# Kernel tuning notes

Hardware: AMD Instinct MI355X
Metric: run time of the kernel (lower is better)

## Reference

```python
import jax, jax.numpy as jnp
import numpy as np

N_PROP = 1000
N_CLS = 81  # includes background class 0
IMG_H, IMG_W = 800, 1333
WX, WY, WW, WH = 10.0, 10.0, 5.0, 5.0
BBOX_XFORM_CLIP = float(np.log(1000.0 / 16.0))
SCORE_THRESH = 0.05
NMS_THRESH = 0.5
DET_PER_IMG = 100


def _decode(box_regression, proposals):
    widths = proposals[:, 2] - proposals[:, 0] + 1.0
    heights = proposals[:, 3] - proposals[:, 1] + 1.0
    ctr_x = proposals[:, 0] + 0.5 * widths
    ctr_y = proposals[:, 1] + 0.5 * heights
    rel = box_regression.reshape(box_regression.shape[0], -1, 4)  # [N, C, 4]
    dx = rel[..., 0] / WX
    dy = rel[..., 1] / WY
    dw = jnp.minimum(rel[..., 2] / WW, BBOX_XFORM_CLIP)
    dh = jnp.minimum(rel[..., 3] / WH, BBOX_XFORM_CLIP)
    pcx = dx * widths[:, None] + ctr_x[:, None]
    pcy = dy * heights[:, None] + ctr_y[:, None]
    pw = jnp.exp(dw) * widths[:, None]
    ph = jnp.exp(dh) * heights[:, None]
    return jnp.stack([pcx - 0.5 * pw, pcy - 0.5 * ph,
                      pcx + 0.5 * pw - 1.0, pcy + 0.5 * ph - 1.0], axis=-1)  # [N, C, 4]


def _clip_boxes(b, h, w):
    x1 = jnp.clip(b[..., 0], 0.0, w - 1.0)
    y1 = jnp.clip(b[..., 1], 0.0, h - 1.0)
    x2 = jnp.clip(b[..., 2], 0.0, w - 1.0)
    y2 = jnp.clip(b[..., 3], 0.0, h - 1.0)
    return jnp.stack([x1, y1, x2, y2], axis=-1)


def _nms_keep(boxes, scores, valid):
    # Greedy NMS for one class. boxes [N,4], scores [N], valid [N].
    # Returns keep mask in the ORIGINAL proposal order.
    n = scores.shape[0]
    order = jnp.argsort(-jnp.where(valid, scores, -jnp.inf))
    b = boxes[order]
    v = valid[order]
    x1, y1, x2, y2 = b[:, 0], b[:, 1], b[:, 2], b[:, 3]
    area = (x2 - x1 + 1.0) * (y2 - y1 + 1.0)
    iw = jnp.clip(jnp.minimum(x2[:, None], x2[None, :]) - jnp.maximum(x1[:, None], x1[None, :]) + 1.0, 0.0)
    ih = jnp.clip(jnp.minimum(y2[:, None], y2[None, :]) - jnp.maximum(y1[:, None], y1[None, :]) + 1.0, 0.0)
    inter = iw * ih
    iou = inter / (area[:, None] + area[None, :] - inter)
    idx = jnp.arange(n)

    def body(i, keep):
        sup = (iou[i] > NMS_THRESH) & (idx > i) & keep[i]
        return keep & ~sup

    keep = jax.lax.fori_loop(0, n, body, v)
    return jnp.zeros(n, dtype=bool).at[order].set(keep)


def _postprocess(class_logits, box_regression, proposal_boxes, image_h, image_w):
    prob = jax.nn.softmax(class_logits, axis=-1)             # [N, C]
    boxes = _decode(box_regression, proposal_boxes)           # [N, C, 4]
    boxes = _clip_boxes(boxes, float(image_h), float(image_w))
    scores_c = prob[:, 1:].T                                  # [C-1, N] skip background
    boxes_c = jnp.transpose(boxes[:, 1:, :], (1, 0, 2))       # [C-1, N, 4]
    valid = scores_c > SCORE_THRESH
    keep = jax.vmap(_nms_keep)(boxes_c, scores_c, valid)      # [C-1, N]
    masked = jnp.where(keep, scores_c, -jnp.inf)
    count = jnp.sum(keep)
    # torch.kthvalue(n - 100) == 101st largest kept score; keep scores >= it
    topv = jax.lax.top_k(masked.reshape(-1), DET_PER_IMG + 1)[0]
    image_thresh = jnp.where(count > DET_PER_IMG, topv[DET_PER_IMG], -jnp.inf)
    final = keep & (masked >= image_thresh)
    c1, n = scores_c.shape
    labels = jnp.broadcast_to(jnp.arange(1, c1 + 1, dtype=jnp.int32)[:, None], (c1, n))
    out_scores = jnp.where(final, scores_c, 0.0).reshape(-1)
    out_boxes = jnp.where(final[..., None], boxes_c, 0.0).reshape(-1, 4)
    out5 = jnp.concatenate([out_boxes, out_scores[:, None]], axis=1)  # [(C-1)*N, 5]
    return out5, jnp.where(final, labels, 0).reshape(-1), final.reshape(-1)


def setup_inputs() -> dict:
    key = jax.random.key(0)
    k1, k2, k3, k4 = jax.random.split(key, 4)
    # scale logits so a realistic fraction of softmax scores clears the 0.05 threshold
    class_logits = 3.0 * jax.random.normal(k1, (N_PROP, N_CLS), dtype=jnp.float32)
    box_regression = jax.random.normal(k2, (N_PROP, N_CLS * 4), dtype=jnp.float32)
    cxy = jax.random.uniform(k3, (N_PROP, 2), dtype=jnp.float32) * jnp.array([IMG_W, IMG_H], jnp.float32)
    wh = 16.0 + 284.0 * jax.random.uniform(k4, (N_PROP, 2), dtype=jnp.float32)
    x1y1 = jnp.clip(cxy - 0.5 * wh, 0.0)
    x2y2 = jnp.minimum(cxy + 0.5 * wh, jnp.array([IMG_W - 1.0, IMG_H - 1.0], jnp.float32))
    proposal_boxes = jnp.concatenate([x1y1, x2y2], axis=1)  # [N, 4] xyxy
    return {"class_logits": class_logits, "box_regression": box_regression,
            "proposal_boxes": proposal_boxes, "image_h": IMG_H, "image_w": IMG_W}


def reference(class_logits, box_regression, proposal_boxes, image_h, image_w):
    return _postprocess(class_logits, box_regression, proposal_boxes, image_h, image_w)
```

## Files before the change

kernel.cpp:

```cpp
#include <hip/hip_runtime.h>
#include <math.h>

#define N_PROP 1000
#define N_CLS  81
#define N_FG   80
#define SCORE_THRESH 0.05f
#define NMS_THRESH   0.5f
#define DET_PER_IMG  100
#define BBOX_CLIP    4.135166556742356f

#define LBL_OFF    400000
#define FIN_OFF    480000


__global__ __launch_bounds__(256)
void softmax_zero_kernel(const float* __restrict__ logits,
                         float* __restrict__ out,
                         int* __restrict__ count,
                         float* __restrict__ probT) {
    const int b = blockIdx.x;
    const int t = threadIdx.x;
    const int lane = t & 63;
    const int wave = t >> 6;
    if (b == 0 && t == 0) *count = 0;

    float4 z = make_float4(0.f, 0.f, 0.f, 0.f);
    float4* o4 = (float4*)out;
    for (int i = b * 256 + t; i < 140000; i += 250 * 256) o4[i] = z;

    const int n = b * 4 + wave;
    if (n < N_PROP) {
        const float* lrow = logits + (size_t)n * N_CLS;
        float v0 = lrow[lane];
        float v1 = (lane + 64 < N_CLS) ? lrow[lane + 64] : -INFINITY;
        float m = fmaxf(v0, v1);
        for (int off = 32; off; off >>= 1) m = fmaxf(m, __shfl_down(m, off));
        m = __shfl(m, 0);
        float e0 = expf(v0 - m);
        float e1 = (lane + 64 < N_CLS) ? expf(v1 - m) : 0.0f;
        float s = e0 + e1;
        for (int off = 32; off; off >>= 1) s += __shfl_down(s, off);
        s = __shfl(s, 0);
        if (lane >= 1)          probT[(size_t)(lane - 1) * N_PROP + n] = e0 / s;
        if (lane + 64 < N_CLS)  probT[(size_t)(lane + 63) * N_PROP + n] = e1 / s;
    }
}

__global__ __launch_bounds__(256)
void nms_kernel(const float* __restrict__ probT,
                const float* __restrict__ props,
                const float* __restrict__ reg,
                const int* __restrict__ ihp,
                const int* __restrict__ iwp,
                float* __restrict__ out,
                int* __restrict__ count,
                float* __restrict__ compact,
                int* __restrict__ svRow) {
    const int c = blockIdx.x;
    const int t = threadIdx.x;
    const int lane = t & 63;
    const int cls = c + 1;
    const unsigned long long lm = (1ull << lane) - 1ull;

    __shared__ float sSc[N_PROP];
    __shared__ int   sIdx[N_PROP];
    __shared__ int   sPos[N_PROP];
    __shared__ float sx1[N_PROP], sy1[N_PROP], sx2[N_PROP], sy2[N_PROP];
    __shared__ float sar[N_PROP], sSc2[N_PROP];
    __shared__ int   sJdx[N_PROP];
    __shared__ unsigned char sKeep[N_PROP];
    __shared__ int   shV;

    for (int j = t; j < N_PROP; j += 256) sSc[j] = probT[(size_t)c * N_PROP + j];
    __syncthreads();

    if (t < 64) {
        int V = 0;
        #pragma unroll
        for (int it = 0; it < 16; ++it) {
            int j = it * 64 + lane;
            float sc = (j < N_PROP) ? sSc[j] : -1.0f;
            bool val = (j < N_PROP) && (sc > SCORE_THRESH);
            unsigned long long mask = __ballot(val);
            if (val) { int p = V + __popcll(mask & lm); sSc[p] = sc; sIdx[p] = j; }
            V += __popcll(mask);
        }
        if (lane == 0) shV = V;
    }
    __syncthreads();
    const int V = shV;

    for (int v = t; v < V; v += 256) {
        float s = sSc[v];
        int id = sIdx[v];
        int r = 0;
        for (int u = 0; u < V; ++u) {
            float su = sSc[u];
            r += (su > s) || (su == s && sIdx[u] < id);
        }
        sPos[v] = r;
    }
    __syncthreads();

    const float W1 = (float)iwp[0] - 1.0f;
    const float H1 = (float)ihp[0] - 1.0f;
    for (int v = t; v < V; v += 256) {
        int r = sPos[v];
        int j = sIdx[v];
        float4 pr = *(const float4*)(props + (size_t)j * 4);
        float w  = pr.z - pr.x + 1.0f;
        float h  = pr.w - pr.y + 1.0f;
        float cx = pr.x + 0.5f * w;
        float cy = pr.y + 0.5f * h;
        float4 rr = *(const float4*)(reg + ((size_t)j * N_CLS + cls) * 4);
        float dx = rr.x / 10.0f;
        float dy = rr.y / 10.0f;
        float dw = fminf(rr.z / 5.0f, BBOX_CLIP);
        float dh = fminf(rr.w / 5.0f, BBOX_CLIP);
        float pcx = dx * w + cx;
        float pcy = dy * h + cy;
        float pw = expf(dw) * w;
        float ph = expf(dh) * h;
        float bx1 = pcx - 0.5f * pw;
        float by1 = pcy - 0.5f * ph;
        float bx2 = pcx + 0.5f * pw - 1.0f;
        float by2 = pcy + 0.5f * ph - 1.0f;
        bx1 = fminf(fmaxf(bx1, 0.0f), W1);
        bx2 = fminf(fmaxf(bx2, 0.0f), W1);
        by1 = fminf(fmaxf(by1, 0.0f), H1);
        by2 = fminf(fmaxf(by2, 0.0f), H1);
        sx1[r] = bx1; sy1[r] = by1; sx2[r] = bx2; sy2[r] = by2;
        sar[r] = (bx2 - bx1 + 1.0f) * (by2 - by1 + 1.0f);
        sSc2[r] = sSc[v];
        sJdx[r] = j;
        sKeep[r] = 1;
    }
    __syncthreads();

    for (int r = 0; r < V; ++r) {
        if (sKeep[r]) {
            const float X1 = sx1[r], Y1 = sy1[r], X2 = sx2[r], Y2 = sy2[r], A = sar[r];
            for (int v = r + 1 + t; v < V; v += 256) {
                if (sKeep[v]) {
                    float iw = fminf(X2, sx2[v]) - fmaxf(X1, sx1[v]) + 1.0f;
                    float ih = fminf(Y2, sy2[v]) - fmaxf(Y1, sy1[v]) + 1.0f;
                    iw = fmaxf(iw, 0.0f);
                    ih = fmaxf(ih, 0.0f);
                    float inter = iw * ih;
                    float iou = inter / (A + sar[v] - inter);
                    if (iou > NMS_THRESH) sKeep[v] = 0;
                }
            }
        }
        __syncthreads();
    }

    for (int vb = 0; vb < V; vb += 256) {
        int v = vb + t;
        bool k = (v < V) && sKeep[v];
        unsigned long long mask = __ballot(k);
        int cntw = __popcll(mask);
        int base = 0;
        if (lane == 0 && cntw > 0) base = atomicAdd(count, cntw);
        base = __shfl(base, 0);
        if (k) {
            int row = c * N_PROP + sJdx[v];
            size_t o = (size_t)row * 5;
            out[o + 0] = sx1[v];
            out[o + 1] = sy1[v];
            out[o + 2] = sx2[v];
            out[o + 3] = sy2[v];
            out[o + 4] = sSc2[v];
            out[LBL_OFF + row] = (float)cls;
            out[FIN_OFF + row] = 1.0f;
            int pos = base + __popcll(mask & lm);
            compact[pos] = sSc2[v];
            svRow[pos] = row;
        }
    }
}

__global__ __launch_bounds__(256)
void finalize_kernel(float* __restrict__ out,
                     const float* __restrict__ compact,
                     const int* __restrict__ svRow,
                     const int* __restrict__ count) {
    __shared__ float lsc[8192];
    __shared__ float sTh;
    const int n = *count;
    const int t = threadIdx.x;
    const int lane = t & 63;

    if (n <= DET_PER_IMG) return;

    const bool useL = (n <= 8192);
    if (useL) {
        for (int i = t; i < n; i += 256) lsc[i] = compact[i];
    }
    __syncthreads();

    if (t < 64) {
        unsigned lo = 0x3D4CCCCCu, hi = 0x40000000u;
        while (hi - lo > 1u) {
            unsigned mid = lo + ((hi - lo) >> 1);
            float mv = __uint_as_float(mid);
            int cnt = 0;
            if (useL) {
                for (int i = lane; i < n; i += 64) cnt += (lsc[i] >= mv) ? 1 : 0;
            } else {
                for (int i = lane; i < n; i += 64) cnt += (compact[i] >= mv) ? 1 : 0;
            }
            for (int off = 32; off; off >>= 1) cnt += __shfl_xor(cnt, off);
            if (cnt >= DET_PER_IMG + 1) lo = mid; else hi = mid;
        }
        if (lane == 0) sTh = __uint_as_float(lo);
    }
    __syncthreads();
    const float th = sTh;

    for (int i = blockIdx.x * 256 + t; i < n; i += gridDim.x * 256) {
        float sc = compact[i];
        if (sc < th) {
            int row = svRow[i];
            size_t o = (size_t)row * 5;
            out[o + 0] = 0.0f;
            out[o + 1] = 0.0f;
            out[o + 2] = 0.0f;
            out[o + 3] = 0.0f;
            out[o + 4] = 0.0f;
            out[LBL_OFF + row] = 0.0f;
            out[FIN_OFF + row] = 0.0f;
        }
    }
}

extern "C" void kernel_launch(void* const* d_in, const int* in_sizes, int n_in,
                              void* d_out, int out_size, void* d_ws, size_t ws_size,
                              hipStream_t stream) {
    const float* logits = (const float*)d_in[0];
    const float* reg    = (const float*)d_in[1];
    const float* props  = (const float*)d_in[2];
    const int*   ihp    = (const int*)d_in[3];
    const int*   iwp    = (const int*)d_in[4];
    float* out = (float*)d_out;

    char* ws = (char*)d_ws;
    int*   count   = (int*)(ws + 0);
    float* probT   = (float*)(ws + 64);
    float* compact = (float*)(ws + 320064);
    int*   svRow   = (int*)(ws + 640064);

    softmax_zero_kernel<<<250, 256, 0, stream>>>(logits, out, count, probT);
    nms_kernel<<<N_FG, 256, 0, stream>>>(probT, props, reg, ihp, iwp,
                                         out, count, compact, svRow);
    finalize_kernel<<<16, 256, 0, stream>>>(out, compact, svRow, count);
}
```

Baseline: 70.28 us.

## Add bitmask-based single-wave NMS fast path for classes with at most 128 candidates

For classes with at most 128 candidates above the score threshold, the kernel now fuses rank computation with box decoding. It precomputes a per-box suppression bitmask against all higher-ranked boxes, then runs greedy NMS inside a single wave using ballots instead of one block-wide barrier per candidate. This removes up to V __syncthreads in the serial NMS loop. The cost is a full triangular IoU computation, done without early skipping of already suppressed boxes. Larger classes fall back to the original path.

```diff
diff --git a/kernel.cpp b/kernel.cpp
--- a/kernel.cpp
+++ b/kernel.cpp
@@ -69,6 +69,7 @@
     __shared__ float sar[N_PROP], sSc2[N_PROP];
     __shared__ int   sJdx[N_PROP];
     __shared__ unsigned char sKeep[N_PROP];
+    __shared__ unsigned long long sColMask[128][2];
     __shared__ int   shV;
 
     for (int j = t; j < N_PROP; j += 256) sSc[j] = probT[(size_t)c * N_PROP + j];
@@ -90,92 +91,190 @@
     __syncthreads();
     const int V = shV;
 
-    for (int v = t; v < V; v += 256) {
-        float s = sSc[v];
-        int id = sIdx[v];
-        int r = 0;
-        for (int u = 0; u < V; ++u) {
-            float su = sSc[u];
-            r += (su > s) || (su == s && sIdx[u] < id);
-        }
-        sPos[v] = r;
-    }
-    __syncthreads();
-
     const float W1 = (float)iwp[0] - 1.0f;
     const float H1 = (float)ihp[0] - 1.0f;
-    for (int v = t; v < V; v += 256) {
-        int r = sPos[v];
-        int j = sIdx[v];
-        float4 pr = *(const float4*)(props + (size_t)j * 4);
-        float w  = pr.z - pr.x + 1.0f;
-        float h  = pr.w - pr.y + 1.0f;
-        float cx = pr.x + 0.5f * w;
-        float cy = pr.y + 0.5f * h;
-        float4 rr = *(const float4*)(reg + ((size_t)j * N_CLS + cls) * 4);
-        float dx = rr.x / 10.0f;
-        float dy = rr.y / 10.0f;
-        float dw = fminf(rr.z / 5.0f, BBOX_CLIP);
-        float dh = fminf(rr.w / 5.0f, BBOX_CLIP);
-        float pcx = dx * w + cx;
-        float pcy = dy * h + cy;
-        float pw = expf(dw) * w;
-        float ph = expf(dh) * h;
-        float bx1 = pcx - 0.5f * pw;
-        float by1 = pcy - 0.5f * ph;
-        float bx2 = pcx + 0.5f * pw - 1.0f;
-        float by2 = pcy + 0.5f * ph - 1.0f;
-        bx1 = fminf(fmaxf(bx1, 0.0f), W1);
-        bx2 = fminf(fmaxf(bx2, 0.0f), W1);
-        by1 = fminf(fmaxf(by1, 0.0f), H1);
-        by2 = fminf(fmaxf(by2, 0.0f), H1);
-        sx1[r] = bx1; sy1[r] = by1; sx2[r] = bx2; sy2[r] = by2;
-        sar[r] = (bx2 - bx1 + 1.0f) * (by2 - by1 + 1.0f);
-        sSc2[r] = sSc[v];
-        sJdx[r] = j;
-        sKeep[r] = 1;
-    }
-    __syncthreads();
-
-    for (int r = 0; r < V; ++r) {
-        if (sKeep[r]) {
-            const float X1 = sx1[r], Y1 = sy1[r], X2 = sx2[r], Y2 = sy2[r], A = sar[r];
-            for (int v = r + 1 + t; v < V; v += 256) {
-                if (sKeep[v]) {
-                    float iw = fminf(X2, sx2[v]) - fmaxf(X1, sx1[v]) + 1.0f;
-                    float ih = fminf(Y2, sy2[v]) - fmaxf(Y1, sy1[v]) + 1.0f;
-                    iw = fmaxf(iw, 0.0f);
-                    ih = fmaxf(ih, 0.0f);
-                    float inter = iw * ih;
-                    float iou = inter / (A + sar[v] - inter);
-                    if (iou > NMS_THRESH) sKeep[v] = 0;
+
+    if (V <= 128) {
+        if (t < V) {
+            float s = sSc[t];
+            int id = sIdx[t];
+            int r = 0;
+            for (int u = 0; u < V; ++u) {
+                float su = sSc[u];
+                r += (su > s) || (su == s && sIdx[u] < id);
+            }
+            float4 pr = *(const float4*)(props + (size_t)id * 4);
+            float w  = pr.z - pr.x + 1.0f;
+            float h  = pr.w - pr.y + 1.0f;
+            float cx = pr.x + 0.5f * w;
+            float cy = pr.y + 0.5f * h;
+            float4 rr = *(const float4*)(reg + ((size_t)id * N_CLS + cls) * 4);
+            float dx = rr.x / 10.0f;
+            float dy = rr.y / 10.0f;
+            float dw = fminf(rr.z / 5.0f, BBOX_CLIP);
+            float dh = fminf(rr.w / 5.0f, BBOX_CLIP);
+            float pcx = dx * w + cx;
+            float pcy = dy * h + cy;
+            float pw = expf(dw) * w;
+            float ph = expf(dh) * h;
+            float bx1 = fminf(fmaxf(pcx - 0.5f * pw, 0.0f), W1);
+            float by1 = fminf(fmaxf(pcy - 0.5f * ph, 0.0f), H1);
+            float bx2 = fminf(fmaxf(pcx + 0.5f * pw - 1.0f, 0.0f), W1);
+            float by2 = fminf(fmaxf(pcy + 0.5f * ph - 1.0f, 0.0f), H1);
+            sx1[r] = bx1; sy1[r] = by1; sx2[r] = bx2; sy2[r] = by2;
+            sar[r] = (bx2 - bx1 + 1.0f) * (by2 - by1 + 1.0f);
+            sSc2[r] = s;
+            sJdx[r] = id;
+        }
+        __syncthreads();
+
+        if (t < V) {
+            const float X1 = sx1[t], Y1 = sy1[t], X2 = sx2[t], Y2 = sy2[t], A = sar[t];
+            unsigned long long m0 = 0ull, m1 = 0ull;
+            for (int r = 0; r < t; ++r) {
+                float iw = fmaxf(fminf(sx2[r], X2) - fmaxf(sx1[r], X1) + 1.0f, 0.0f);
+                float ih = fmaxf(fminf(sy2[r], Y2) - fmaxf(sy1[r], Y1) + 1.0f, 0.0f);
+                float inter = iw * ih;
+                float iou = inter / (sar[r] + A - inter);
+                if (iou > NMS_THRESH) {
+                    if (r < 64) m0 |= 1ull << r; else m1 |= 1ull << (r - 64);
                 }
             }
+            sColMask[t][0] = m0;
+            sColMask[t][1] = m1;
         }
         __syncthreads();
-    }
-
-    for (int vb = 0; vb < V; vb += 256) {
-        int v = vb + t;
-        bool k = (v < V) && sKeep[v];
-        unsigned long long mask = __ballot(k);
-        int cntw = __popcll(mask);
-        int base = 0;
-        if (lane == 0 && cntw > 0) base = atomicAdd(count, cntw);
-        base = __shfl(base, 0);
-        if (k) {
-            int row = c * N_PROP + sJdx[v];
-            size_t o = (size_t)row * 5;
-            out[o + 0] = sx1[v];
-            out[o + 1] = sy1[v];
-            out[o + 2] = sx2[v];
-            out[o + 3] = sy2[v];
-            out[o + 4] = sSc2[v];
-            out[LBL_OFF + row] = (float)cls;
-            out[FIN_OFF + row] = 1.0f;
-            int pos = base + __popcll(mask & lm);
-            compact[pos] = sSc2[v];
-            svRow[pos] = row;
+
+        if (t < 64) {
+            const bool hasA = (lane < V), hasB = (64 + lane < V);
+            unsigned long long Mlo = 0ull, M2lo = 0ull, M2hi = 0ull;
+            if (hasA) Mlo  = sColMask[lane][0];
+            if (hasB) { M2lo = sColMask[64 + lane][0]; M2hi = sColMask[64 + lane][1]; }
+
+            unsigned long long keep = 0ull, keep2 = 0ull;
+            bool a = hasA, a2 = hasB;
+            while (true) {
+                unsigned long long b1 = __ballot(a);
+                unsigned long long b2 = __ballot(a2);
+                if (!(b1 | b2)) break;
+                int r = b1 ? (__ffsll((long long)b1) - 1) : (64 + __ffsll((long long)b2) - 1);
+                if (r < 64) {
+                    keep |= 1ull << r;
+                    if (a  && ((Mlo  >> r) & 1ull)) a  = false;
+                    if (a2 && ((M2lo >> r) & 1ull)) a2 = false;
+                    if (lane == r) a = false;
+                } else {
+                    int rr = r - 64;
+                    keep2 |= 1ull << rr;
+                    if (a2 && ((M2hi >> rr) & 1ull)) a2 = false;
+                    if (lane == rr) a2 = false;
+                }
+            }
+
+            int total = __popcll(keep) + __popcll(keep2);
+            int base = 0;
+            if (lane == 0 && total > 0) base = atomicAdd(count, total);
+            base = __shfl(base, 0);
+            if ((keep >> lane) & 1ull) {
+                float sc = sSc2[lane];
+                int row = c * N_PROP + sJdx[lane];
+                size_t o = (size_t)row * 5;
+                out[o + 0] = sx1[lane]; out[o + 1] = sy1[lane];
+                out[o + 2] = sx2[lane]; out[o + 3] = sy2[lane];
+                out[o + 4] = sc;
+                out[LBL_OFF + row] = (float)cls;
+                out[FIN_OFF + row] = 1.0f;
+                int pos = base + __popcll(keep & lm);
+                compact[pos] = sc; svRow[pos] = row;
+            }
+            if ((keep2 >> lane) & 1ull) {
+                float sc = sSc2[64 + lane];
+                int row = c * N_PROP + sJdx[64 + lane];
+                size_t o = (size_t)row * 5;
+                out[o + 0] = sx1[64 + lane]; out[o + 1] = sy1[64 + lane];
+                out[o + 2] = sx2[64 + lane]; out[o + 3] = sy2[64 + lane];
+                out[o + 4] = sc;
+                out[LBL_OFF + row] = (float)cls;
+                out[FIN_OFF + row] = 1.0f;
+                int pos = base + __popcll(keep) + __popcll(keep2 & lm);
+                compact[pos] = sc; svRow[pos] = row;
+            }
+        }
+    } else {
+        for (int v = t; v < V; v += 256) {
+            float s = sSc[v];
+            int id = sIdx[v];
+            int r = 0;
+            for (int u = 0; u < V; ++u) {
+                float su = sSc[u];
+                r += (su > s) || (su == s && sIdx[u] < id);
+            }
+            sPos[v] = r;
+        }
+        __syncthreads();
+        for (int v = t; v < V; v += 256) {
+            int r = sPos[v];
+            int j = sIdx[v];
+            float4 pr = *(const float4*)(props + (size_t)j * 4);
+            float w  = pr.z - pr.x + 1.0f;
+            float h  = pr.w - pr.y + 1.0f;
+            float cx = pr.x + 0.5f * w;
+            float cy = pr.y + 0.5f * h;
+            float4 rr = *(const float4*)(reg + ((size_t)j * N_CLS + cls) * 4);
+            float dx = rr.x / 10.0f;
+            float dy = rr.y / 10.0f;
+            float dw = fminf(rr.z / 5.0f, BBOX_CLIP);
+            float dh = fminf(rr.w / 5.0f, BBOX_CLIP);
+            float pcx = dx * w + cx;
+            float pcy = dy * h + cy;
+            float pw = expf(dw) * w;
+            float ph = expf(dh) * h;
+            float bx1 = fminf(fmaxf(pcx - 0.5f * pw, 0.0f), W1);
+            float by1 = fminf(fmaxf(pcy - 0.5f * ph, 0.0f), H1);
+            float bx2 = fminf(fmaxf(pcx + 0.5f * pw - 1.0f, 0.0f), W1);
+            float by2 = fminf(fmaxf(pcy + 0.5f * ph - 1.0f, 0.0f), H1);
+            sx1[r] = bx1; sy1[r] = by1; sx2[r] = bx2; sy2[r] = by2;
+            sar[r] = (bx2 - bx1 + 1.0f) * (by2 - by1 + 1.0f);
+            sSc2[r] = sSc[v];
+            sJdx[r] = j;
+            sKeep[r] = 1;
+        }
+        __syncthreads();
+        for (int r = 0; r < V; ++r) {
+            if (sKeep[r]) {
+                const float X1 = sx1[r], Y1 = sy1[r], X2 = sx2[r], Y2 = sy2[r], A = sar[r];
+                for (int v = r + 1 + t; v < V; v += 256) {
+                    if (sKeep[v]) {
+                        float iw = fmaxf(fminf(X2, sx2[v]) - fmaxf(X1, sx1[v]) + 1.0f, 0.0f);
+                        float ih = fmaxf(fminf(Y2, sy2[v]) - fmaxf(Y1, sy1[v]) + 1.0f, 0.0f);
+                        float inter = iw * ih;
+                        float iou = inter / (A + sar[v] - inter);
+                        if (iou > NMS_THRESH) sKeep[v] = 0;
+                    }
+                }
+            }
+            __syncthreads();
+        }
+        for (int vb = 0; vb < V; vb += 256) {
+            int v = vb + t;
+            bool k = (v < V) && sKeep[v];
+            unsigned long long mask = __ballot(k);
+            int cntw = __popcll(mask);
+            int base = 0;
+            if (lane == 0 && cntw > 0) base = atomicAdd(count, cntw);
+            base = __shfl(base, 0);
+            if (k) {
+                int row = c * N_PROP + sJdx[v];
+                size_t o = (size_t)row * 5;
+                out[o + 0] = sx1[v]; out[o + 1] = sy1[v];
+                out[o + 2] = sx2[v]; out[o + 3] = sy2[v];
+                out[o + 4] = sSc2[v];
+                out[LBL_OFF + row] = (float)cls;
+                out[FIN_OFF + row] = 1.0f;
+                int pos = base + __popcll(mask & lm);
+                compact[pos] = sSc2[v];
+                svRow[pos] = row;
+            }
         }
     }
 }
```

Result: faster. 66.96 us (median of 2 runs) (-4.7%).
